# Optimization experiments

Hardware: AMD Instinct MI355X
Metric: run time of the kernel (lower is better)

## Reference

```python
import jax, jax.numpy as jnp
import numpy as np

NEG_SLOPE = 0.2  # PyG GATConv default negative_slope
LN_EPS = 1e-5


def gat_conv(x, edge, W, a_src, a_dst, bias, concat):
    """PyG-style GATConv. edge: [2, E] (src, dst), self-loops already included."""
    H, C = a_src.shape
    n = x.shape[0]
    xh = (x @ W).reshape(n, H, C)                      # [N, H, C]
    es = jnp.einsum('nhc,hc->nh', xh, a_src)           # [N, H]
    ed = jnp.einsum('nhc,hc->nh', xh, a_dst)           # [N, H]
    src, dst = edge[0], edge[1]
    e = jax.nn.leaky_relu(es[src] + ed[dst], NEG_SLOPE)  # [E, H]
    m = jax.ops.segment_max(e, dst, num_segments=n)      # [N, H]
    m = jnp.where(jnp.isfinite(m), m, 0.0)
    w = jnp.exp(e - m[dst])                              # [E, H]
    denom = jax.ops.segment_sum(w, dst, num_segments=n)  # [N, H] (>0: self-loops)
    alpha = w / denom[dst]                               # [E, H]
    out = jax.ops.segment_sum(alpha[:, :, None] * xh[src], dst, num_segments=n)  # [N,H,C]
    out = out.reshape(n, H * C) if concat else out.mean(axis=1)
    return out + bias


def layer_norm(x, g, b):
    mu = x.mean(axis=-1, keepdims=True)
    var = ((x - mu) ** 2).mean(axis=-1, keepdims=True)
    return (x - mu) * jax.lax.rsqrt(var + LN_EPS) * g + b


def setup_inputs() -> dict:
    key = jax.random.key(0)
    ks = jax.random.split(key, 12)
    N, D_IN, HID, OUT, H = 100000, 256, 256, 64, 8
    C1 = HID // H  # 32
    E = 1600000
    x = jax.random.normal(ks[0], (N, D_IN), dtype=jnp.float32)
    edge_index = jax.random.randint(ks[1], (2, E), 0, N, dtype=jnp.int64)
    s = 0.05
    return {
        'x': x,
        'edge_index': edge_index,
        'W1': jax.random.normal(ks[2], (D_IN, HID), jnp.float32) * s,
        'a_src1': jax.random.normal(ks[3], (H, C1), jnp.float32) * s,
        'a_dst1': jax.random.normal(ks[4], (H, C1), jnp.float32) * s,
        'b1': jnp.zeros((HID,), jnp.float32),
        'g1': jnp.ones((HID,), jnp.float32),
        'be1': jnp.zeros((HID,), jnp.float32),
        'W2': jax.random.normal(ks[5], (HID, OUT), jnp.float32) * s,
        'a_src2': jax.random.normal(ks[6], (1, OUT), jnp.float32) * s,
        'a_dst2': jax.random.normal(ks[7], (1, OUT), jnp.float32) * s,
        'b2': jnp.zeros((OUT,), jnp.float32),
        'g2': jnp.ones((OUT,), jnp.float32),
        'be2': jnp.zeros((OUT,), jnp.float32),
    }


def reference(x, edge_index, W1, a_src1, a_dst1, b1, g1, be1, W2, a_src2, a_dst2, b2, g2, be2):
    # eval mode: dropout_edge and F.dropout are identity
    n = x.shape[0]
    loops = jnp.arange(n, dtype=edge_index.dtype)
    edge = jnp.concatenate([edge_index, jnp.stack([loops, loops])], axis=1)  # add self-loops
    h = gat_conv(x, edge, W1, a_src1, a_dst1, b1, concat=True)
    h = jax.nn.relu(layer_norm(h, g1, be1))
    h = gat_conv(h, edge, W2, a_src2, a_dst2, b2, concat=False)
    h = layer_norm(h, g2, be2)
    return jax.nn.log_softmax(h, axis=1)
```

## Files before the change

### kernel.cpp

```cpp
#include <hip/hip_runtime.h>
#include <math.h>

#define LRELU(v) ((v) > 0.0f ? (v) : 0.2f * (v))

typedef __bf16 bf16x8 __attribute__((ext_vector_type(8)));
typedef float f32x4 __attribute__((ext_vector_type(4)));
typedef float f32x2 __attribute__((ext_vector_type(2)));

__device__ __forceinline__ unsigned short f2bf(float f) {
    unsigned int u = __float_as_uint(f);
    u += 0x7FFF + ((u >> 16) & 1);
    return (unsigned short)(u >> 16);
}
__device__ __forceinline__ float bf2f(unsigned short s) {
    return __uint_as_float(((unsigned int)s) << 16);
}

__global__ __launch_bounds__(256) void prep_k(const float* __restrict__ W1, unsigned short* __restrict__ W1T,
                                              const float* __restrict__ W2, unsigned short* __restrict__ W2T,
                                              const int* __restrict__ edge, int* __restrict__ cnt,
                                              int* __restrict__ rank, int E) {
    int b = blockIdx.x;
    if (b < 256) {
        int i = b * 256 + threadIdx.x;
        int k = i >> 8, n = i & 255;
        W1T[(size_t)n * 256 + k] = f2bf(W1[i]);
    } else if (b < 320) {
        int i = (b - 256) * 256 + threadIdx.x;
        int k = i >> 6, n = i & 63;
        W2T[(size_t)n * 256 + k] = f2bf(W2[i]);
    } else {
        int i = (b - 320) * 256 + threadIdx.x;
        if (i < E) rank[i] = atomicAdd(&cnt[edge[E + i]], 1);
    }
}

__global__ __launch_bounds__(256) void psum_k(const int* __restrict__ cnt, int* __restrict__ bsum, int N) {
    __shared__ int wsh[4];
    int b = blockIdx.x;
    int gi = b * 1024 + threadIdx.x * 4;
    int s = 0;
    if (gi + 3 < N) {
        int4 v = *(const int4*)(cnt + gi);
        s = v.x + v.y + v.z + v.w + 4;
    } else {
        for (int j = 0; j < 4; ++j) if (gi + j < N) s += cnt[gi + j] + 1;
    }
#pragma unroll
    for (int off = 1; off < 64; off <<= 1) s += __shfl_xor(s, off, 64);
    if ((threadIdx.x & 63) == 0) wsh[threadIdx.x >> 6] = s;
    __syncthreads();
    if (threadIdx.x == 0) bsum[b] = wsh[0] + wsh[1] + wsh[2] + wsh[3];
}

__global__ void bscan_k(int* __restrict__ bsum, int B) {
    __shared__ int sh[128];
    int t = threadIdx.x;
    int v = (t < B) ? bsum[t] : 0;
    sh[t] = v;
    __syncthreads();
    for (int off = 1; off < 128; off <<= 1) {
        int u = (t >= off) ? sh[t - off] : 0;
        __syncthreads();
        sh[t] += u;
        __syncthreads();
    }
    if (t < B) bsum[t] = sh[t] - v;
}

__global__ __launch_bounds__(256) void rowptr_k(const int* __restrict__ cnt, const int* __restrict__ bsum,
                                                int* __restrict__ row_ptr, int N) {
    __shared__ int wsh[4];
    int b = blockIdx.x;
    int t = threadIdx.x;
    int gi = b * 1024 + t * 4;
    int c[4];
    int s = 0;
#pragma unroll
    for (int j = 0; j < 4; ++j) {
        int i = gi + j;
        c[j] = (i < N) ? cnt[i] + 1 : 0;
        s += c[j];
    }
    int lane = t & 63, w = t >> 6;
    int ps = s;
#pragma unroll
    for (int off = 1; off < 64; off <<= 1) {
        int u = __shfl_up(ps, off, 64);
        if (lane >= off) ps += u;
    }
    if (lane == 63) wsh[w] = ps;
    __syncthreads();
    int wbase = 0;
    for (int k = 0; k < w; ++k) wbase += wsh[k];
    int base = bsum[b] + wbase + (ps - s);
#pragma unroll
    for (int j = 0; j < 4; ++j) {
        int i = gi + j;
        if (i < N) row_ptr[i] = base;
        base += c[j];
    }
    if (N - 1 >= gi && N - 1 < gi + 4) row_ptr[N] = base;
}

__global__ void scatter_k(const int* __restrict__ edge, const int* __restrict__ row_ptr,
                          const int* __restrict__ rank, int* __restrict__ col, int E, int N) {
    int i = blockIdx.x * blockDim.x + threadIdx.x;
    if (i < E) {
        int dst = edge[E + i];
        col[row_ptr[dst] + rank[i]] = edge[i];
    } else if (i < E + N) {
        int n = i - E;
        col[row_ptr[n + 1] - 1] = n;
    }
}

__global__ __launch_bounds__(256) void gemm1f_k(const float* __restrict__ A,
                                                const unsigned short* __restrict__ BT,
                                                unsigned char* __restrict__ Q, int M) {
    constexpr int K = 256, BM = 128, BK = 32;
    __shared__ char As[BM * 80];
    __shared__ char Bs[256 * 80];
    int tid = threadIdx.x;
    int m0 = blockIdx.x * BM;
    int wid = tid >> 6, lane = tid & 63;
    int wm = (wid >> 1) * 64, wn = (wid & 1) * 128;
    int l15 = lane & 15, g = lane >> 4;
    f32x4 acc[4][8] = {};

    for (int k0 = 0; k0 < K; k0 += BK) {
#pragma unroll
        for (int i = 0; i < 2; ++i) {
            int c = tid + i * 256;
            int r = c >> 2, kc = c & 3;
            int gm = m0 + r; if (gm >= M) gm = M - 1;
            const float* src = A + (size_t)gm * K + k0 + kc * 8;
            float4 v0 = *(const float4*)(src);
            float4 v1 = *(const float4*)(src + 4);
            uint4 pk;
            pk.x = f2bf(v0.x) | ((unsigned)f2bf(v0.y) << 16);
            pk.y = f2bf(v0.z) | ((unsigned)f2bf(v0.w) << 16);
            pk.z = f2bf(v1.x) | ((unsigned)f2bf(v1.y) << 16);
            pk.w = f2bf(v1.z) | ((unsigned)f2bf(v1.w) << 16);
            *(uint4*)(As + r * 80 + kc * 16) = pk;
        }
#pragma unroll
        for (int i = 0; i < 4; ++i) {
            int c = tid + i * 256;
            int r = c >> 2, kc = c & 3;
            float4 v = *(const float4*)(BT + (size_t)r * K + k0 + kc * 8);
            *(float4*)(Bs + r * 80 + kc * 16) = v;
        }
        __syncthreads();
        bf16x8 af[4], bfr[8];
#pragma unroll
        for (int i = 0; i < 4; ++i)
            af[i] = *(const bf16x8*)(As + (wm + i * 16 + l15) * 80 + g * 16);
#pragma unroll
        for (int j = 0; j < 8; ++j)
            bfr[j] = *(const bf16x8*)(Bs + (wn + j * 16 + l15) * 80 + g * 16);
#pragma unroll
        for (int i = 0; i < 4; ++i)
#pragma unroll
            for (int j = 0; j < 8; ++j)
                acc[i][j] = __builtin_amdgcn_mfma_f32_16x16x32_bf16(af[i], bfr[j], acc[i][j], 0, 0, 0);
        __syncthreads();
    }
#pragma unroll
    for (int i = 0; i < 4; ++i)
#pragma unroll
        for (int j = 0; j < 8; ++j) {
            int col = wn + j * 16 + l15;
            int gmb = m0 + wm + i * 16 + g * 4;
            int p01 = __builtin_amdgcn_cvt_pk_fp8_f32(acc[i][j][0], acc[i][j][1], 0, false);
            int p23 = __builtin_amdgcn_cvt_pk_fp8_f32(acc[i][j][2], acc[i][j][3], 0, false);
#pragma unroll
            for (int r = 0; r < 4; ++r) {
                int gm = gmb + r;
                if (gm < M) {
                    int pk = (r < 2) ? p01 : p23;
                    Q[(size_t)gm * 256 + col] = (unsigned char)((pk >> ((r & 1) * 8)) & 0xff);
                }
            }
        }
}

__global__ __launch_bounds__(256) void gemm2_k(const unsigned short* __restrict__ A,
                                               const unsigned short* __restrict__ BT,
                                               unsigned short* __restrict__ C,
                                               int M, int N, int K) {
    constexpr int BM = 128, BK = 32, BN = 64;
    __shared__ char As[BM * 80];
    __shared__ char Bs[BN * 80];
    int tid = threadIdx.x;
    int m0 = blockIdx.x * BM;
    int wid = tid >> 6, lane = tid & 63;
    int wm = (wid >> 1) * 64, wn = (wid & 1) * 32;
    int l15 = lane & 15, g = lane >> 4;
    f32x4 acc[4][2] = {};

    for (int k0 = 0; k0 < K; k0 += BK) {
#pragma unroll
        for (int i = 0; i < 2; ++i) {
            int c = tid + i * 256;
            int r = c >> 2, kc = c & 3;
            int gm = m0 + r; if (gm >= M) gm = M - 1;
            float4 v = *(const float4*)(A + (size_t)gm * K + k0 + kc * 8);
            *(float4*)(As + r * 80 + kc * 16) = v;
        }
        {
            int c = tid;
            int r = c >> 2, kc = c & 3;
            float4 v = *(const float4*)(BT + (size_t)r * K + k0 + kc * 8);
            *(float4*)(Bs + r * 80 + kc * 16) = v;
        }
        __syncthreads();
        bf16x8 af[4], bfr[2];
#pragma unroll
        for (int i = 0; i < 4; ++i)
            af[i] = *(const bf16x8*)(As + (wm + i * 16 + l15) * 80 + g * 16);
#pragma unroll
        for (int j = 0; j < 2; ++j)
            bfr[j] = *(const bf16x8*)(Bs + (wn + j * 16 + l15) * 80 + g * 16);
#pragma unroll
        for (int i = 0; i < 4; ++i)
#pragma unroll
            for (int j = 0; j < 2; ++j)
                acc[i][j] = __builtin_amdgcn_mfma_f32_16x16x32_bf16(af[i], bfr[j], acc[i][j], 0, 0, 0);
        __syncthreads();
    }
#pragma unroll
    for (int i = 0; i < 4; ++i)
#pragma unroll
        for (int j = 0; j < 2; ++j)
#pragma unroll
            for (int r = 0; r < 4; ++r) {
                int gm = m0 + wm + i * 16 + g * 4 + r;
                if (gm < M)
                    C[(size_t)gm * N + wn + j * 16 + l15] = f2bf(acc[i][j][r]);
            }
}

__global__ void dots1_k(const unsigned char* __restrict__ xq, const float* __restrict__ as_,
                        const float* __restrict__ ad_, float* __restrict__ es,
                        float* __restrict__ ed, int N8) {
    __shared__ float ws[256], wd[256];
    ws[threadIdx.x] = as_[threadIdx.x];
    wd[threadIdx.x] = ad_[threadIdx.x];
    __syncthreads();
    int idx = blockIdx.x * 256 + threadIdx.x;
    if (idx >= N8) return;
    int n = idx >> 3, hh = idx & 7;
    const uint4* p = (const uint4*)(xq + (size_t)n * 256 + hh * 32);
    const float* s = ws + hh * 32;
    const float* d = wd + hh * 32;
    float a = 0.f, b = 0.f;
#pragma unroll
    for (int j = 0; j < 2; ++j) {
        uint4 v = p[j];
        unsigned dws[4] = {v.x, v.y, v.z, v.w};
#pragma unroll
        for (int k = 0; k < 4; ++k) {
            int c0 = j * 16 + k * 4;
            f32x2 lo = __builtin_amdgcn_cvt_pk_f32_fp8(dws[k], false);
            f32x2 hi = __builtin_amdgcn_cvt_pk_f32_fp8(dws[k], true);
            a += lo[0] * s[c0] + lo[1] * s[c0 + 1] + hi[0] * s[c0 + 2] + hi[1] * s[c0 + 3];
            b += lo[0] * d[c0] + lo[1] * d[c0 + 1] + hi[0] * d[c0 + 2] + hi[1] * d[c0 + 3];
        }
    }
    es[idx] = a;
    ed[idx] = b;
}

__global__ void dots2_k(const unsigned short* __restrict__ xh2, const float* __restrict__ as_,
                        const float* __restrict__ ad_, float* __restrict__ es,
                        float* __restrict__ ed, int N) {
    __shared__ float ws[64], wd[64];
    if (threadIdx.x < 64) { ws[threadIdx.x] = as_[threadIdx.x]; wd[threadIdx.x] = ad_[threadIdx.x]; }
    __syncthreads();
    int n = blockIdx.x * blockDim.x + threadIdx.x;
    if (n >= N) return;
    const ushort4* p = (const ushort4*)(xh2 + (size_t)n * 64);
    float a = 0.f, b = 0.f;
#pragma unroll
    for (int j = 0; j < 16; ++j) {
        ushort4 v = p[j];
        a += bf2f(v.x) * ws[j * 4 + 0] + bf2f(v.y) * ws[j * 4 + 1] +
             bf2f(v.z) * ws[j * 4 + 2] + bf2f(v.w) * ws[j * 4 + 3];
        b += bf2f(v.x) * wd[j * 4 + 0] + bf2f(v.y) * wd[j * 4 + 1] +
             bf2f(v.z) * wd[j * 4 + 2] + bf2f(v.w) * wd[j * 4 + 3];
    }
    es[n] = a;
    ed[n] = b;
}

__global__ __launch_bounds__(256) void agg1_k(const unsigned char* __restrict__ xq,
                                              const float* __restrict__ es, const float* __restrict__ ed,
                                              const int* __restrict__ row_ptr, const int* __restrict__ col,
                                              const float* __restrict__ bias, const float* __restrict__ gam,
                                              const float* __restrict__ bet,
                                              unsigned short* __restrict__ hout, int N) {
    int tid = threadIdx.x, wid = tid >> 6, lane = tid & 63;
    int node = blockIdx.x * 4 + wid;
    if (node >= N) return;
    int half = lane >> 5, li = lane & 31, hh = li >> 2;
    int start = row_ptr[node];
    int deg = row_ptr[node + 1] - start;
    float edh = ed[node * 8 + hh];
    f32x2 acc2[4] = {};
    float wsum = 0.f;

    float esA = 0.f, esB = 0.f, esC = 0.f;
    uint2 xA = {0, 0}, xB = {0, 0}, xC = {0, 0};
    int e = half;
    if (e < deg) { int src = col[start + e];
        esA = es[src * 8 + hh]; xA = *(const uint2*)(xq + (size_t)src * 256 + li * 8); }
    if (e + 2 < deg) { int src = col[start + e + 2];
        esB = es[src * 8 + hh]; xB = *(const uint2*)(xq + (size_t)src * 256 + li * 8); }
    if (e + 4 < deg) { int src = col[start + e + 4];
        esC = es[src * 8 + hh]; xC = *(const uint2*)(xq + (size_t)src * 256 + li * 8); }

#define AGG1_STEP(ESB, XB)                                                        \
    {                                                                             \
        float wgt = __expf(LRELU(ESB + edh));                                     \
        wsum += wgt;                                                              \
        f32x2 w2 = {wgt, wgt};                                                    \
        acc2[0] += w2 * __builtin_amdgcn_cvt_pk_f32_fp8(XB.x, false);             \
        acc2[1] += w2 * __builtin_amdgcn_cvt_pk_f32_fp8(XB.x, true);              \
        acc2[2] += w2 * __builtin_amdgcn_cvt_pk_f32_fp8(XB.y, false);             \
        acc2[3] += w2 * __builtin_amdgcn_cvt_pk_f32_fp8(XB.y, true);              \
        if (e + 6 < deg) {                                                        \
            int src = col[start + e + 6];                                         \
            ESB = es[src * 8 + hh];                                               \
            XB = *(const uint2*)(xq + (size_t)src * 256 + li * 8);                \
        }                                                                         \
        e += 2;                                                                   \
    }

    if (e < deg) {
        for (;;) {
            AGG1_STEP(esA, xA);
            if (e >= deg) break;
            AGG1_STEP(esB, xB);
            if (e >= deg) break;
            AGG1_STEP(esC, xC);
            if (e >= deg) break;
        }
    }
#undef AGG1_STEP

    float a8[8];
#pragma unroll
    for (int k = 0; k < 4; ++k) { a8[2 * k] = acc2[k][0]; a8[2 * k + 1] = acc2[k][1]; }
#pragma unroll
    for (int j = 0; j < 8; ++j) a8[j] += __shfl_xor(a8[j], 32, 64);
    wsum += __shfl_xor(wsum, 32, 64);
    float inv = 1.f / wsum;
    float4 bA = *(const float4*)(bias + li * 8);
    float4 bB = *(const float4*)(bias + li * 8 + 4);
    float v[8];
    v[0] = a8[0] * inv + bA.x; v[1] = a8[1] * inv + bA.y;
    v[2] = a8[2] * inv + bA.z; v[3] = a8[3] * inv + bA.w;
    v[4] = a8[4] * inv + bB.x; v[5] = a8[5] * inv + bB.y;
    v[6] = a8[6] * inv + bB.z; v[7] = a8[7] * inv + bB.w;
    float s = 0.f, q = 0.f;
#pragma unroll
    for (int j = 0; j < 8; ++j) { s += v[j]; q += v[j] * v[j]; }
#pragma unroll
    for (int off = 1; off < 32; off <<= 1) { s += __shfl_xor(s, off, 64); q += __shfl_xor(q, off, 64); }
    float mu = s * (1.f / 256.f);
    float var = q * (1.f / 256.f) - mu * mu;
    float rs = rsqrtf(var + 1e-5f);
    float4 gA = *(const float4*)(gam + li * 8);
    float4 gB = *(const float4*)(gam + li * 8 + 4);
    float4 eA = *(const float4*)(bet + li * 8);
    float4 eB = *(const float4*)(bet + li * 8 + 4);
    float o0 = fmaxf((v[0] - mu) * rs * gA.x + eA.x, 0.f);
    float o1 = fmaxf((v[1] - mu) * rs * gA.y + eA.y, 0.f);
    float o2 = fmaxf((v[2] - mu) * rs * gA.z + eA.z, 0.f);
    float o3 = fmaxf((v[3] - mu) * rs * gA.w + eA.w, 0.f);
    float o4 = fmaxf((v[4] - mu) * rs * gB.x + eB.x, 0.f);
    float o5 = fmaxf((v[5] - mu) * rs * gB.y + eB.y, 0.f);
    float o6 = fmaxf((v[6] - mu) * rs * gB.z + eB.z, 0.f);
    float o7 = fmaxf((v[7] - mu) * rs * gB.w + eB.w, 0.f);
    if (half == 0) {
        uint4 pk;
        pk.x = f2bf(o0) | ((unsigned)f2bf(o1) << 16);
        pk.y = f2bf(o2) | ((unsigned)f2bf(o3) << 16);
        pk.z = f2bf(o4) | ((unsigned)f2bf(o5) << 16);
        pk.w = f2bf(o6) | ((unsigned)f2bf(o7) << 16);
        *(uint4*)(hout + (size_t)node * 256 + li * 8) = pk;
    }
}

__global__ __launch_bounds__(256) void agg2_k(const unsigned short* __restrict__ xh2,
                                              const float* __restrict__ es, const float* __restrict__ ed,
                                              const int* __restrict__ row_ptr, const int* __restrict__ col,
                                              const float* __restrict__ bias, const float* __restrict__ gam,
                                              const float* __restrict__ bet,
                                              float* __restrict__ out, int N) {
    int tid = threadIdx.x, wid = tid >> 6, lane = tid & 63;
    int node = blockIdx.x * 4 + wid;
    if (node >= N) return;
    int g = lane >> 3, li = lane & 7;
    int start = row_ptr[node];
    int deg = row_ptr[node + 1] - start;
    float edh = ed[node];
    f32x2 acc2[4] = {};
    float wsum = 0.f;

    float esA = 0.f, esB = 0.f, esC = 0.f;
    uint4 xA = {0, 0, 0, 0}, xB = {0, 0, 0, 0}, xC = {0, 0, 0, 0};
    int e = g;
    if (e < deg) { int src = col[start + e];
        esA = es[src]; xA = *(const uint4*)(xh2 + (size_t)src * 64 + li * 8); }
    if (e + 8 < deg) { int src = col[start + e + 8];
        esB = es[src]; xB = *(const uint4*)(xh2 + (size_t)src * 64 + li * 8); }
    if (e + 16 < deg) { int src = col[start + e + 16];
        esC = es[src]; xC = *(const uint4*)(xh2 + (size_t)src * 64 + li * 8); }

#define AGG2_STEP(ESB, XB)                                                        \
    {                                                                             \
        float wgt = __expf(LRELU(ESB + edh));                                     \
        wsum += wgt;                                                              \
        f32x2 w2 = {wgt, wgt};                                                    \
        f32x2 t0 = {__uint_as_float(XB.x << 16), __uint_as_float(XB.x & 0xffff0000u)}; \
        f32x2 t1 = {__uint_as_float(XB.y << 16), __uint_as_float(XB.y & 0xffff0000u)}; \
        f32x2 t2 = {__uint_as_float(XB.z << 16), __uint_as_float(XB.z & 0xffff0000u)}; \
        f32x2 t3 = {__uint_as_float(XB.w << 16), __uint_as_float(XB.w & 0xffff0000u)}; \
        acc2[0] += w2 * t0;                                                       \
        acc2[1] += w2 * t1;                                                       \
        acc2[2] += w2 * t2;                                                       \
        acc2[3] += w2 * t3;                                                       \
        if (e + 24 < deg) {                                                       \
            int src = col[start + e + 24];                                        \
            ESB = es[src];                                                        \
            XB = *(const uint4*)(xh2 + (size_t)src * 64 + li * 8);                \
        }                                                                         \
        e += 8;                                                                   \
    }

    if (e < deg) {
        for (;;) {
            AGG2_STEP(esA, xA);
            if (e >= deg) break;
            AGG2_STEP(esB, xB);
            if (e >= deg) break;
            AGG2_STEP(esC, xC);
            if (e >= deg) break;
        }
    }
#undef AGG2_STEP

    float a8[8];
#pragma unroll
    for (int k = 0; k < 4; ++k) { a8[2 * k] = acc2[k][0]; a8[2 * k + 1] = acc2[k][1]; }
#pragma unroll
    for (int off = 8; off < 64; off <<= 1) {
#pragma unroll
        for (int j = 0; j < 8; ++j) a8[j] += __shfl_xor(a8[j], off, 64);
        wsum += __shfl_xor(wsum, off, 64);
    }
    int c = li * 8;
    float inv = 1.f / wsum;
    float v[8];
#pragma unroll
    for (int j = 0; j < 8; ++j) v[j] = a8[j] * inv + bias[c + j];
    float s = 0.f, q = 0.f;
#pragma unroll
    for (int j = 0; j < 8; ++j) { s += v[j]; q += v[j] * v[j]; }
#pragma unroll
    for (int off = 1; off < 8; off <<= 1) { s += __shfl_xor(s, off, 64); q += __shfl_xor(q, off, 64); }
    float mu = s * (1.f / 64.f);
    float var = q * (1.f / 64.f) - mu * mu;
    float rs = rsqrtf(var + 1e-5f);
    float o[8];
    float mx = -1e30f;
#pragma unroll
    for (int j = 0; j < 8; ++j) {
        o[j] = (v[j] - mu) * rs * gam[c + j] + bet[c + j];
        mx = fmaxf(mx, o[j]);
    }
#pragma unroll
    for (int off = 1; off < 8; off <<= 1) mx = fmaxf(mx, __shfl_xor(mx, off, 64));
    float se = 0.f;
#pragma unroll
    for (int j = 0; j < 8; ++j) se += __expf(o[j] - mx);
#pragma unroll
    for (int off = 1; off < 8; off <<= 1) se += __shfl_xor(se, off, 64);
    float lse = mx + logf(se);
    if (g == 0) {
        float4 o0 = make_float4(o[0] - lse, o[1] - lse, o[2] - lse, o[3] - lse);
        float4 o1 = make_float4(o[4] - lse, o[5] - lse, o[6] - lse, o[7] - lse);
        *(float4*)(out + (size_t)node * 64 + c) = o0;
        *(float4*)(out + (size_t)node * 64 + c + 4) = o1;
    }
}

extern "C" void kernel_launch(void* const* d_in, const int* in_sizes, int n_in,
                              void* d_out, int out_size, void* d_ws, size_t ws_size,
                              hipStream_t stream) {
    const float* x   = (const float*)d_in[0];
    const int*   edge = (const int*)d_in[1];
    const float* W1  = (const float*)d_in[2];
    const float* as1 = (const float*)d_in[3];
    const float* ad1 = (const float*)d_in[4];
    const float* b1  = (const float*)d_in[5];
    const float* g1  = (const float*)d_in[6];
    const float* be1 = (const float*)d_in[7];
    const float* W2  = (const float*)d_in[8];
    const float* as2 = (const float*)d_in[9];
    const float* ad2 = (const float*)d_in[10];
    const float* b2  = (const float*)d_in[11];
    const float* g2  = (const float*)d_in[12];
    const float* be2 = (const float*)d_in[13];

    int NN = in_sizes[0] / 256;
    int E  = in_sizes[1] / 2;
    int ET = E + NN;

    char* w = (char*)d_ws;
    size_t off = 0;
    auto nxt = [&](size_t b) -> void* {
        void* p = w + off;
        off = (off + b + 255) & ~(size_t)255;
        return p;
    };
    unsigned short* W1T  = (unsigned short*)nxt(256 * 256 * 2);
    unsigned short* W2T  = (unsigned short*)nxt(64 * 256 * 2);
    unsigned char*  xq   = (unsigned char*)nxt((size_t)NN * 256);
    unsigned short* hbuf = (unsigned short*)nxt((size_t)NN * 256 * 2);
    unsigned short* xh2b = (unsigned short*)nxt((size_t)NN * 64 * 2);
    float* es1   = (float*)nxt((size_t)NN * 8 * 4);
    float* ed1   = (float*)nxt((size_t)NN * 8 * 4);
    float* es2   = (float*)nxt((size_t)NN * 4);
    float* ed2   = (float*)nxt((size_t)NN * 4);
    int* row_ptr = (int*)nxt((size_t)(NN + 1) * 4);
    int* tmpN    = (int*)nxt((size_t)NN * 4);
    int* rank    = (int*)nxt((size_t)E * 4);
    int* col     = (int*)nxt((size_t)ET * 4);
    int* bsum    = (int*)nxt(1024 * 4);
    (void)ws_size; (void)n_in; (void)out_size;

    int NB = (NN + 1023) / 1024;

    (void)hipMemsetAsync(tmpN, 0, (size_t)NN * 4, stream);
    prep_k<<<320 + (E + 255) / 256, 256, 0, stream>>>(W1, W1T, W2, W2T, edge, tmpN, rank, E);
    psum_k<<<NB, 256, 0, stream>>>(tmpN, bsum, NN);
    bscan_k<<<1, 128, 0, stream>>>(bsum, NB);
    rowptr_k<<<NB, 256, 0, stream>>>(tmpN, bsum, row_ptr, NN);
    scatter_k<<<(ET + 255) / 256, 256, 0, stream>>>(edge, row_ptr, rank, col, E, NN);

    gemm1f_k<<<(NN + 127) / 128, 256, 0, stream>>>(x, W1T, xq, NN);
    dots1_k<<<(NN * 8 + 255) / 256, 256, 0, stream>>>(xq, as1, ad1, es1, ed1, NN * 8);
    agg1_k<<<(NN + 3) / 4, 256, 0, stream>>>(xq, es1, ed1, row_ptr, col, b1, g1, be1, hbuf, NN);

    gemm2_k<<<(NN + 127) / 128, 256, 0, stream>>>(hbuf, W2T, xh2b, NN, 64, 256);
    dots2_k<<<(NN + 255) / 256, 256, 0, stream>>>(xh2b, as2, ad2, es2, ed2, NN);
    agg2_k<<<(NN + 3) / 4, 256, 0, stream>>>(xh2b, es2, ed2, row_ptr, col, b2, g2, be2,
                                             (float*)d_out, NN);
}
```

Before: 357.1 us.

## Fuse attention dot products into GEMM epilogues and use 32-bit gather addressing

Computes the per-head source/destination attention scores directly from the fp32 MFMA accumulators in both GEMM epilogues, using cross-lane shuffles and a shared-memory reduction, and removes the separate dots1/dots2 kernels. This avoids re-reading the quantized feature matrices and saves two launches. It also changes the scores to come from unquantized accumulators, which slightly alters numerics. Separately, the aggregation gathers now compute addresses with 32-bit shifts and ORs instead of size_t multiplies.

```diff
diff --git a/kernel.cpp b/kernel.cpp
--- a/kernel.cpp
+++ b/kernel.cpp
@@ -117,11 +117,16 @@
 
 __global__ __launch_bounds__(256) void gemm1f_k(const float* __restrict__ A,
                                                 const unsigned short* __restrict__ BT,
-                                                unsigned char* __restrict__ Q, int M) {
+                                                const float* __restrict__ AS1, const float* __restrict__ AD1,
+                                                unsigned char* __restrict__ Q,
+                                                float* __restrict__ es1, float* __restrict__ ed1, int M) {
     constexpr int K = 256, BM = 128, BK = 32;
     __shared__ char As[BM * 80];
     __shared__ char Bs[256 * 80];
+    __shared__ float sa[256], sd_[256];
     int tid = threadIdx.x;
+    sa[tid] = AS1[tid];
+    sd_[tid] = AD1[tid];
     int m0 = blockIdx.x * BM;
     int wid = tid >> 6, lane = tid & 63;
     int wm = (wid >> 1) * 64, wn = (wid & 1) * 128;
@@ -183,16 +188,48 @@
                 }
             }
         }
+#pragma unroll
+    for (int i = 0; i < 4; ++i)
+#pragma unroll
+        for (int r = 0; r < 4; ++r) {
+            float pes[4], ped[4];
+#pragma unroll
+            for (int h = 0; h < 4; ++h) {
+                int c0 = wn + (2 * h) * 16 + l15;
+                int c1 = wn + (2 * h + 1) * 16 + l15;
+                pes[h] = acc[i][2 * h][r] * sa[c0] + acc[i][2 * h + 1][r] * sa[c1];
+                ped[h] = acc[i][2 * h][r] * sd_[c0] + acc[i][2 * h + 1][r] * sd_[c1];
+            }
+#pragma unroll
+            for (int off = 1; off < 16; off <<= 1) {
+#pragma unroll
+                for (int h = 0; h < 4; ++h) {
+                    pes[h] += __shfl_xor(pes[h], off, 64);
+                    ped[h] += __shfl_xor(ped[h], off, 64);
+                }
+            }
+            if (l15 == 0) {
+                int gm = m0 + wm + i * 16 + g * 4 + r;
+                if (gm < M) {
+                    *(float4*)(es1 + (size_t)gm * 8 + 4 * (wid & 1)) = make_float4(pes[0], pes[1], pes[2], pes[3]);
+                    *(float4*)(ed1 + (size_t)gm * 8 + 4 * (wid & 1)) = make_float4(ped[0], ped[1], ped[2], ped[3]);
+                }
+            }
+        }
 }
 
 __global__ __launch_bounds__(256) void gemm2_k(const unsigned short* __restrict__ A,
                                                const unsigned short* __restrict__ BT,
+                                               const float* __restrict__ AS2, const float* __restrict__ AD2,
                                                unsigned short* __restrict__ C,
-                                               int M, int N, int K) {
-    constexpr int BM = 128, BK = 32, BN = 64;
+                                               float* __restrict__ es2, float* __restrict__ ed2, int M) {
+    constexpr int N = 64, K = 256, BM = 128, BK = 32, BN = 64;
     __shared__ char As[BM * 80];
     __shared__ char Bs[BN * 80];
+    __shared__ float s2a[64], s2d[64];
+    __shared__ float red[128][2][2];
     int tid = threadIdx.x;
+    if (tid < 64) { s2a[tid] = AS2[tid]; s2d[tid] = AD2[tid]; }
     int m0 = blockIdx.x * BM;
     int wid = tid >> 6, lane = tid & 63;
     int wm = (wid >> 1) * 64, wn = (wid & 1) * 32;
@@ -239,59 +276,32 @@
                 if (gm < M)
                     C[(size_t)gm * N + wn + j * 16 + l15] = f2bf(acc[i][j][r]);
             }
-}
-
-__global__ void dots1_k(const unsigned char* __restrict__ xq, const float* __restrict__ as_,
-                        const float* __restrict__ ad_, float* __restrict__ es,
-                        float* __restrict__ ed, int N8) {
-    __shared__ float ws[256], wd[256];
-    ws[threadIdx.x] = as_[threadIdx.x];
-    wd[threadIdx.x] = ad_[threadIdx.x];
+#pragma unroll
+    for (int i = 0; i < 4; ++i)
+#pragma unroll
+        for (int r = 0; r < 4; ++r) {
+            int c0 = wn + l15, c1 = wn + 16 + l15;
+            float pe = acc[i][0][r] * s2a[c0] + acc[i][1][r] * s2a[c1];
+            float pd = acc[i][0][r] * s2d[c0] + acc[i][1][r] * s2d[c1];
+#pragma unroll
+            for (int off = 1; off < 16; off <<= 1) {
+                pe += __shfl_xor(pe, off, 64);
+                pd += __shfl_xor(pd, off, 64);
+            }
+            if (l15 == 0) {
+                int rl = wm + i * 16 + g * 4 + r;
+                red[rl][wid & 1][0] = pe;
+                red[rl][wid & 1][1] = pd;
+            }
+        }
     __syncthreads();
-    int idx = blockIdx.x * 256 + threadIdx.x;
-    if (idx >= N8) return;
-    int n = idx >> 3, hh = idx & 7;
-    const uint4* p = (const uint4*)(xq + (size_t)n * 256 + hh * 32);
-    const float* s = ws + hh * 32;
-    const float* d = wd + hh * 32;
-    float a = 0.f, b = 0.f;
-#pragma unroll
-    for (int j = 0; j < 2; ++j) {
-        uint4 v = p[j];
-        unsigned dws[4] = {v.x, v.y, v.z, v.w};
-#pragma unroll
-        for (int k = 0; k < 4; ++k) {
-            int c0 = j * 16 + k * 4;
-            f32x2 lo = __builtin_amdgcn_cvt_pk_f32_fp8(dws[k], false);
-            f32x2 hi = __builtin_amdgcn_cvt_pk_f32_fp8(dws[k], true);
-            a += lo[0] * s[c0] + lo[1] * s[c0 + 1] + hi[0] * s[c0 + 2] + hi[1] * s[c0 + 3];
-            b += lo[0] * d[c0] + lo[1] * d[c0 + 1] + hi[0] * d[c0 + 2] + hi[1] * d[c0 + 3];
-        }
-    }
-    es[idx] = a;
-    ed[idx] = b;
-}
-
-__global__ void dots2_k(const unsigned short* __restrict__ xh2, const float* __restrict__ as_,
-                        const float* __restrict__ ad_, float* __restrict__ es,
-                        float* __restrict__ ed, int N) {
-    __shared__ float ws[64], wd[64];
-    if (threadIdx.x < 64) { ws[threadIdx.x] = as_[threadIdx.x]; wd[threadIdx.x] = ad_[threadIdx.x]; }
-    __syncthreads();
-    int n = blockIdx.x * blockDim.x + threadIdx.x;
-    if (n >= N) return;
-    const ushort4* p = (const ushort4*)(xh2 + (size_t)n * 64);
-    float a = 0.f, b = 0.f;
-#pragma unroll
-    for (int j = 0; j < 16; ++j) {
-        ushort4 v = p[j];
-        a += bf2f(v.x) * ws[j * 4 + 0] + bf2f(v.y) * ws[j * 4 + 1] +
-             bf2f(v.z) * ws[j * 4 + 2] + bf2f(v.w) * ws[j * 4 + 3];
-        b += bf2f(v.x) * wd[j * 4 + 0] + bf2f(v.y) * wd[j * 4 + 1] +
-             bf2f(v.z) * wd[j * 4 + 2] + bf2f(v.w) * wd[j * 4 + 3];
-    }
-    es[n] = a;
-    ed[n] = b;
+    if (tid < 128) {
+        int gm = m0 + tid;
+        if (gm < M) {
+            es2[gm] = red[tid][0][0] + red[tid][1][0];
+            ed2[gm] = red[tid][0][1] + red[tid][1][1];
+        }
+    }
 }
 
 __global__ __launch_bounds__(256) void agg1_k(const unsigned char* __restrict__ xq,
@@ -303,22 +313,24 @@
     int tid = threadIdx.x, wid = tid >> 6, lane = tid & 63;
     int node = blockIdx.x * 4 + wid;
     if (node >= N) return;
-    int half = lane >> 5, li = lane & 31, hh = li >> 2;
+    int half = lane >> 5, li = lane & 31;
+    unsigned hh = (unsigned)(li >> 2);
+    unsigned lib = (unsigned)(li * 8);
     int start = row_ptr[node];
     int deg = row_ptr[node + 1] - start;
-    float edh = ed[node * 8 + hh];
+    float edh = ed[((unsigned)node << 3) + hh];
     f32x2 acc2[4] = {};
     float wsum = 0.f;
 
     float esA = 0.f, esB = 0.f, esC = 0.f;
     uint2 xA = {0, 0}, xB = {0, 0}, xC = {0, 0};
     int e = half;
-    if (e < deg) { int src = col[start + e];
-        esA = es[src * 8 + hh]; xA = *(const uint2*)(xq + (size_t)src * 256 + li * 8); }
-    if (e + 2 < deg) { int src = col[start + e + 2];
-        esB = es[src * 8 + hh]; xB = *(const uint2*)(xq + (size_t)src * 256 + li * 8); }
-    if (e + 4 < deg) { int src = col[start + e + 4];
-        esC = es[src * 8 + hh]; xC = *(const uint2*)(xq + (size_t)src * 256 + li * 8); }
+    if (e < deg) { unsigned src = (unsigned)col[start + e];
+        esA = es[(src << 3) + hh]; xA = *(const uint2*)(xq + ((src << 8) | lib)); }
+    if (e + 2 < deg) { unsigned src = (unsigned)col[start + e + 2];
+        esB = es[(src << 3) + hh]; xB = *(const uint2*)(xq + ((src << 8) | lib)); }
+    if (e + 4 < deg) { unsigned src = (unsigned)col[start + e + 4];
+        esC = es[(src << 3) + hh]; xC = *(const uint2*)(xq + ((src << 8) | lib)); }
 
 #define AGG1_STEP(ESB, XB)                                                        \
     {                                                                             \
@@ -330,9 +342,9 @@
         acc2[2] += w2 * __builtin_amdgcn_cvt_pk_f32_fp8(XB.y, false);             \
         acc2[3] += w2 * __builtin_amdgcn_cvt_pk_f32_fp8(XB.y, true);              \
         if (e + 6 < deg) {                                                        \
-            int src = col[start + e + 6];                                         \
-            ESB = es[src * 8 + hh];                                               \
-            XB = *(const uint2*)(xq + (size_t)src * 256 + li * 8);                \
+            unsigned src = (unsigned)col[start + e + 6];                          \
+            ESB = es[(src << 3) + hh];                                            \
+            XB = *(const uint2*)(xq + ((src << 8) | lib));                        \
         }                                                                         \
         e += 2;                                                                   \
     }
@@ -403,6 +415,7 @@
     int node = blockIdx.x * 4 + wid;
     if (node >= N) return;
     int g = lane >> 3, li = lane & 7;
+    unsigned lib = (unsigned)(li * 8);
     int start = row_ptr[node];
     int deg = row_ptr[node + 1] - start;
     float edh = ed[node];
@@ -412,12 +425,12 @@
     float esA = 0.f, esB = 0.f, esC = 0.f;
     uint4 xA = {0, 0, 0, 0}, xB = {0, 0, 0, 0}, xC = {0, 0, 0, 0};
     int e = g;
-    if (e < deg) { int src = col[start + e];
-        esA = es[src]; xA = *(const uint4*)(xh2 + (size_t)src * 64 + li * 8); }
-    if (e + 8 < deg) { int src = col[start + e + 8];
-        esB = es[src]; xB = *(const uint4*)(xh2 + (size_t)src * 64 + li * 8); }
-    if (e + 16 < deg) { int src = col[start + e + 16];
-        esC = es[src]; xC = *(const uint4*)(xh2 + (size_t)src * 64 + li * 8); }
+    if (e < deg) { unsigned src = (unsigned)col[start + e];
+        esA = es[src]; xA = *(const uint4*)(xh2 + ((src << 6) | lib)); }
+    if (e + 8 < deg) { unsigned src = (unsigned)col[start + e + 8];
+        esB = es[src]; xB = *(const uint4*)(xh2 + ((src << 6) | lib)); }
+    if (e + 16 < deg) { unsigned src = (unsigned)col[start + e + 16];
+        esC = es[src]; xC = *(const uint4*)(xh2 + ((src << 6) | lib)); }
 
 #define AGG2_STEP(ESB, XB)                                                        \
     {                                                                             \
@@ -433,9 +446,9 @@
         acc2[2] += w2 * t2;                                                       \
         acc2[3] += w2 * t3;                                                       \
         if (e + 24 < deg) {                                                       \
-            int src = col[start + e + 24];                                        \
+            unsigned src = (unsigned)col[start + e + 24];                         \
             ESB = es[src];                                                        \
-            XB = *(const uint4*)(xh2 + (size_t)src * 64 + li * 8);                \
+            XB = *(const uint4*)(xh2 + ((src << 6) | lib));                       \
         }                                                                         \
         e += 8;                                                                   \
     }
@@ -551,12 +564,10 @@
     rowptr_k<<<NB, 256, 0, stream>>>(tmpN, bsum, row_ptr, NN);
     scatter_k<<<(ET + 255) / 256, 256, 0, stream>>>(edge, row_ptr, rank, col, E, NN);
 
-    gemm1f_k<<<(NN + 127) / 128, 256, 0, stream>>>(x, W1T, xq, NN);
-    dots1_k<<<(NN * 8 + 255) / 256, 256, 0, stream>>>(xq, as1, ad1, es1, ed1, NN * 8);
+    gemm1f_k<<<(NN + 127) / 128, 256, 0, stream>>>(x, W1T, as1, ad1, xq, es1, ed1, NN);
     agg1_k<<<(NN + 3) / 4, 256, 0, stream>>>(xq, es1, ed1, row_ptr, col, b1, g1, be1, hbuf, NN);
 
-    gemm2_k<<<(NN + 127) / 128, 256, 0, stream>>>(hbuf, W2T, xh2b, NN, 64, 256);
-    dots2_k<<<(NN + 255) / 256, 256, 0, stream>>>(xh2b, as2, ad2, es2, ed2, NN);
+    gemm2_k<<<(NN + 127) / 128, 256, 0, stream>>>(hbuf, W2T, as2, ad2, xh2b, es2, ed2, NN);
     agg2_k<<<(NN + 3) / 4, 256, 0, stream>>>(xh2b, es2, ed2, row_ptr, col, b2, g2, be2,
                                              (float*)d_out, NN);
 }
```

Result: slower. 376.3 us (+5.4%).
